# Kernel tuning notes

Measured on AMD Instinct MI355X. Metric: run time of the kernel, lower is better.

## Reference

```python
import jax, jax.numpy as jnp
import numpy as np

EMB = 1024
NHEAD = 16
HEAD_DIM = EMB // NHEAD  # 64
L = 2048
NEG = -1e30


def setup_inputs() -> dict:
    key = jax.random.key(0)
    ks = jax.random.split(key, 8)
    # xavier_uniform bound for square [EMB, EMB] matrices
    bound = float(np.sqrt(6.0 / (EMB + EMB)))
    def xavier(k):
        return jax.random.uniform(k, (EMB, EMB), jnp.float32, -bound, bound)
    return {
        "q": jax.random.normal(ks[0], (L, EMB), jnp.float32),
        "k": jax.random.normal(ks[1], (L, EMB), jnp.float32),
        "v": jax.random.normal(ks[2], (L, EMB), jnp.float32),
        "mask": jax.random.randint(ks[3], (NHEAD, L, L), 0, 2) > 0,
        "Wq": xavier(ks[4]),
        "Wk": xavier(ks[5]),
        "Wv": xavier(ks[6]),
        "Wo": xavier(ks[7]),
    }


def reference(q, k, v, mask, Wq, Wk, Wv, Wo):
    scaling = HEAD_DIM ** -0.5
    # F.linear(x, W) = x @ W.T ; reshape to [H, L, D]
    Q = (q @ Wq.T).reshape(L, NHEAD, HEAD_DIM).swapaxes(0, 1)
    K = (k @ Wk.T).reshape(L, NHEAD, HEAD_DIM).swapaxes(0, 1)
    V = (v @ Wv.T).reshape(L, NHEAD, HEAD_DIM).swapaxes(0, 1)
    scores = jnp.einsum("hld,hmd->hlm", Q, K) * scaling  # [H, L, L]
    scores = jnp.where(mask, jnp.asarray(NEG, scores.dtype), scores)
    p = jax.nn.softmax(scores, axis=-1)
    # attn_mask=True: multiplicative re-mask after softmax (custom path)
    p = p * (~mask).astype(p.dtype)
    # dropout is a no-op in eval mode
    attn_out = jnp.einsum("hlm,hmd->hld", p, V)  # [H, L, D]
    attn_out = attn_out.swapaxes(0, 1).reshape(L, EMB)
    return attn_out @ Wo.T
```

## Files before the change

kernel.cpp:

```cpp
#include <hip/hip_runtime.h>
#include <stdint.h>

#define EMB   1024
#define NHEAD 16
#define HDIM  64
#define SEQ   2048

typedef unsigned short ushort_t;
typedef unsigned int   uint32;
typedef __attribute__((ext_vector_type(8))) short bfrag;
typedef __attribute__((ext_vector_type(4))) float ffrag;

#define MFMA(a, b, c) __builtin_amdgcn_mfma_f32_16x16x32_bf16((a), (b), (c), 0, 0, 0)

__device__ inline ushort_t f2bf(float f) {
  uint32 u = __float_as_uint(f);
  u += 0x7FFFu + ((u >> 16) & 1u);
  return (ushort_t)(u >> 16);
}
__device__ inline uint32 pack2(float a, float b) {
  return (uint32)f2bf(a) | ((uint32)f2bf(b) << 16);
}

__device__ inline void glds16(const ushort_t* g, ushort_t* l) {
  __builtin_amdgcn_global_load_lds(
      (const __attribute__((address_space(1))) uint32*)(uintptr_t)g,
      (__attribute__((address_space(3))) uint32*)(uintptr_t)l, 16, 0, 0);
}

__global__ void detect_mask_kernel(const uint32* __restrict__ mw, int* __restrict__ flag) {
  uint32 w = mw[threadIdx.x];
  bool is4 = (w == 0u) || (w == 1u) || (w == 0x3F800000u);
  unsigned long long bad = __ballot(!is4);
  if (threadIdx.x == 0) flag[0] = (bad == 0ull) ? 1 : 0;
}

__global__ __launch_bounds__(256) void compress_mask(
    const void* __restrict__ maskp, const int* __restrict__ flag, ushort_t* __restrict__ bm)
{
  size_t t = (size_t)blockIdx.x * 256 + threadIdx.x;
  size_t row = t >> 7;
  int c16 = (int)(t & 127);
  size_t base = row * SEQ + (size_t)c16 * 16;
  ushort_t mv = 0;
  if (*flag) {
    const uint4* p = (const uint4*)((const uint32*)maskp + base);
    uint4 a0 = p[0], a1 = p[1], a2 = p[2], a3 = p[3];
    uint32 aw[16] = {a0.x,a0.y,a0.z,a0.w, a1.x,a1.y,a1.z,a1.w,
                     a2.x,a2.y,a2.z,a2.w, a3.x,a3.y,a3.z,a3.w};
    #pragma unroll
    for (int i = 0; i < 16; ++i) mv |= (ushort_t)((aw[i] != 0u) ? 1u : 0u) << i;
  } else {
    uint4 b0 = *(const uint4*)((const unsigned char*)maskp + base);
    uint32 bw[4] = {b0.x, b0.y, b0.z, b0.w};
    #pragma unroll
    for (int i = 0; i < 16; ++i)
      mv |= (ushort_t)((((bw[i >> 2] >> ((i & 3) * 8)) & 0xFFu) != 0u) ? 1u : 0u) << i;
  }
  bm[t] = mv;
}

__global__ __launch_bounds__(256) void cvt_all(
    const float4* __restrict__ q,  const float4* __restrict__ k,  const float4* __restrict__ v,
    const float4* __restrict__ wq, const float4* __restrict__ wk, const float4* __restrict__ wv,
    const float4* __restrict__ wo,
    uint2* __restrict__ qb,  uint2* __restrict__ kb,  uint2* __restrict__ vb,
    uint2* __restrict__ wqb, uint2* __restrict__ wkb, uint2* __restrict__ wvb,
    uint2* __restrict__ wob)
{
  int t = blockIdx.x * 256 + threadIdx.x;
  int s = blockIdx.y;
  const float4* src; uint2* dst; int n4;
  switch (s) {
    case 0: src = q;  dst = qb;  n4 = (SEQ * EMB) / 4; break;
    case 1: src = k;  dst = kb;  n4 = (SEQ * EMB) / 4; break;
    case 2: src = v;  dst = vb;  n4 = (SEQ * EMB) / 4; break;
    case 3: src = wq; dst = wqb; n4 = (EMB * EMB) / 4; break;
    case 4: src = wk; dst = wkb; n4 = (EMB * EMB) / 4; break;
    case 5: src = wv; dst = wvb; n4 = (EMB * EMB) / 4; break;
    default: src = wo; dst = wob; n4 = (EMB * EMB) / 4; break;
  }
  if (t >= n4) return;
  float4 f = src[t];
  uint2 o; o.x = pack2(f.x, f.y); o.y = pack2(f.z, f.w);
  dst[t] = o;
}

template<int MODE, int BN>
__device__ inline void gemm_body(const ushort_t* A, const ushort_t* B, void* Cp,
                                 int m0, int n0, ushort_t* As, ushort_t* Bs) {
  const int tid = threadIdx.x, lane = tid & 63, w = tid >> 6;
  const int wm = (w >> 1) * 64, wn = (w & 1) * (BN / 2);
  const int col = lane & 15, g = lane >> 4;
  constexpr int TN = BN / 32;
  constexpr int BIT = BN / 32;
  constexpr int ASZ = 128 * 64;
  constexpr int BSZ = BN * 64;

  ffrag acc[4][TN] = {};

  auto stage = [&](int kt, int buf) {
    const int k0 = kt * 64;
    ushort_t* Ad = As + buf * ASZ;
    ushort_t* Bd = Bs + buf * BSZ;
    #pragma unroll
    for (int it = 0; it < 4; ++it) {
      int p = it * 256 + tid;
      int row = p >> 3, pc = p & 7;
      glds16(A + (size_t)(m0 + row) * EMB + k0 + (pc ^ (row & 7)) * 8, &Ad[p * 8]);
    }
    #pragma unroll
    for (int it = 0; it < BIT; ++it) {
      int p = it * 256 + tid;
      int row = p >> 3, pc = p & 7;
      glds16(B + (size_t)(n0 + row) * EMB + k0 + (pc ^ (row & 7)) * 8, &Bd[p * 8]);
    }
  };

  stage(0, 0);

  for (int kt = 0; kt < 16; ++kt) {
    const int buf = kt & 1;
    __syncthreads();
    if (kt < 15) stage(kt + 1, buf ^ 1);

    const ushort_t* Ac = As + buf * ASZ;
    const ushort_t* Bc = Bs + buf * BSZ;

    #pragma unroll
    for (int c = 0; c < 2; ++c) {
      bfrag av[4], bv[TN];
      #pragma unroll
      for (int t = 0; t < 4; ++t) {
        int ra = wm + t * 16 + col;
        av[t] = *(const bfrag*)&Ac[ra * 64 + ((c * 4 + g) ^ (ra & 7)) * 8];
      }
      #pragma unroll
      for (int t = 0; t < TN; ++t) {
        int rb = wn + t * 16 + col;
        bv[t] = *(const bfrag*)&Bc[rb * 64 + ((c * 4 + g) ^ (rb & 7)) * 8];
      }
      #pragma unroll
      for (int tm = 0; tm < 4; ++tm)
        #pragma unroll
        for (int tn = 0; tn < TN; ++tn)
          acc[tm][tn] = MFMA(av[tm], bv[tn], acc[tm][tn]);
    }
  }

  const int rbase = g * 4;
  #pragma unroll
  for (int tm = 0; tm < 4; ++tm)
    #pragma unroll
    for (int tn = 0; tn < TN; ++tn)
      #pragma unroll
      for (int r = 0; r < 4; ++r) {
        int m = m0 + wm + tm * 16 + rbase + r;
        int n = n0 + wn + tn * 16 + col;
        float vv = acc[tm][tn][r];
        if (MODE == 0) {
          ((ushort_t*)Cp)[((size_t)(n >> 6) * SEQ + m) * HDIM + (n & 63)] = f2bf(vv);
        } else if (MODE == 1) {
          ((ushort_t*)Cp)[((size_t)(m >> 6) * HDIM + (m & 63)) * SEQ + n] = f2bf(vv);
        } else {
          ((float*)Cp)[(size_t)m * EMB + n] = vv;
        }
      }
}

__global__ __launch_bounds__(256) void gemm_qkv(
    const ushort_t* __restrict__ qb, const ushort_t* __restrict__ kb, const ushort_t* __restrict__ vb,
    const ushort_t* __restrict__ Wqb, const ushort_t* __restrict__ Wkb, const ushort_t* __restrict__ Wvb,
    ushort_t* __restrict__ Qb, ushort_t* __restrict__ Kb, ushort_t* __restrict__ Vtb)
{
  __shared__ ushort_t As[2 * 128 * 64];
  __shared__ ushort_t Bs[2 * 64 * 64];
  const int z = blockIdx.y, bid = blockIdx.x;
  if (z == 0) {
    gemm_body<0, 64>(qb, Wqb, Qb, (bid >> 4) * 128, (bid & 15) * 64, As, Bs);
  } else if (z == 1) {
    gemm_body<0, 64>(kb, Wkb, Kb, (bid >> 4) * 128, (bid & 15) * 64, As, Bs);
  } else {
    gemm_body<1, 64>(Wvb, vb, Vtb, (bid >> 5) * 128, (bid & 31) * 64, As, Bs);
  }
}

__global__ __launch_bounds__(256) void gemm_out(
    const ushort_t* __restrict__ A, const ushort_t* __restrict__ B, float* __restrict__ C)
{
  __shared__ ushort_t As[2 * 128 * 64];
  __shared__ ushort_t Bs[2 * 64 * 64];
  gemm_body<2, 64>(A, B, (void*)C, blockIdx.y * 128, blockIdx.x * 64, As, Bs);
}

__global__ __launch_bounds__(256) void attn_mfma(
    const ushort_t* __restrict__ Qb,
    const ushort_t* __restrict__ Kb,
    const ushort_t* __restrict__ Vtb,
    const ushort_t* __restrict__ bm,
    ushort_t* __restrict__ attnb)
{
  __shared__ ushort_t Ks[2][2][64 * 64];
  __shared__ ushort_t Vs[2][64 * 64];
  __shared__ ushort_t Ps[4][16 * 72];

  const int tid  = threadIdx.x;
  const int lane = tid & 63;
  const int w    = tid >> 6;
  const int h    = blockIdx.y;
  const int l0   = blockIdx.x * 64;
  const int col  = lane & 15, g = lane >> 4, kg8 = g * 8, rbase = g * 4;

  ushort_t* pw = &Ps[w][0];

  {
    int rl = lane >> 2, seg = (lane & 3) * 16;
    const uint4* pq = (const uint4*)(Qb + ((size_t)h * SEQ + l0 + w * 16 + rl) * HDIM + seg);
    uint4 q0 = pq[0], q1 = pq[1];
    *(uint4*)&pw[rl * 72 + seg] = q0;
    *(uint4*)&pw[rl * 72 + seg + 8] = q1;
  }
  bfrag qf[2];
  qf[0] = *(const bfrag*)&pw[col * 72 + kg8];
  qf[1] = *(const bfrag*)&pw[col * 72 + 32 + kg8];

  auto stage_k = [&](int t2, int buf) {
    const int cb = t2 * 128;
    #pragma unroll
    for (int it = 0; it < 2; ++it) {
      int p = it * 256 + tid;
      int row = p >> 3, pc = p & 7;
      int sc = (pc ^ (row & 7)) * 8;
      glds16(Kb + ((size_t)h * SEQ + cb + row) * HDIM + sc,      &Ks[buf][0][p * 8]);
      glds16(Kb + ((size_t)h * SEQ + cb + 64 + row) * HDIM + sc, &Ks[buf][1][p * 8]);
    }
  };
  auto stage_v = [&](int t2) {
    const int cb = t2 * 128;
    #pragma unroll
    for (int it = 0; it < 2; ++it) {
      int p = it * 256 + tid;
      int row = p >> 3, pc = p & 7;
      int sc = (pc ^ (row & 7)) * 8;
      glds16(Vtb + ((size_t)h * HDIM + row) * SEQ + cb + sc,      &Vs[0][p * 8]);
      glds16(Vtb + ((size_t)h * HDIM + row) * SEQ + cb + 64 + sc, &Vs[1][p * 8]);
    }
  };

  stage_k(0, 0);
  stage_v(0);
  __syncthreads();

  const size_t bmbase = ((size_t)h * SEQ + l0 + w * 16 + col) * 128 + g;
  ushort_t mvn0 = bm[bmbase];
  ushort_t mvn1 = bm[bmbase + 4];

  float lsum = 0.f;
  ffrag oacc[4] = {};

  for (int t = 0; t < 16; ++t) {
    const int buf = t & 1;
    if (t < 15) stage_k(t + 1, buf ^ 1);

    int mv0 = (int)mvn0, mv1 = (int)mvn1;
    if (t < 15) {
      mvn0 = bm[bmbase + (size_t)(t + 1) * 8];
      mvn1 = bm[bmbase + (size_t)(t + 1) * 8 + 4];
    }

    ffrag s0[4] = {}, s1[4] = {};
    #pragma unroll
    for (int c = 0; c < 2; ++c)
      #pragma unroll
      for (int tn = 0; tn < 4; ++tn) {
        int row = tn * 16 + col;
        int sw = ((c * 4 + g) ^ (row & 7)) * 8;
        bfrag kf0 = *(const bfrag*)&Ks[buf][0][row * 64 + sw];
        bfrag kf1 = *(const bfrag*)&Ks[buf][1][row * 64 + sw];
        s0[tn] = MFMA(kf0, qf[c], s0[tn]);
        s1[tn] = MFMA(kf1, qf[c], s1[tn]);
      }

    #pragma unroll
    for (int tn = 0; tn < 4; ++tn) {
      int m16 = __shfl(mv0, tn * 16 + col, 64);
      float p0 = ((m16 >> (rbase + 0)) & 1) ? 0.f : __expf(s0[tn][0] * 0.125f);
      float p1 = ((m16 >> (rbase + 1)) & 1) ? 0.f : __expf(s0[tn][1] * 0.125f);
      float p2 = ((m16 >> (rbase + 2)) & 1) ? 0.f : __expf(s0[tn][2] * 0.125f);
      float p3 = ((m16 >> (rbase + 3)) & 1) ? 0.f : __expf(s0[tn][3] * 0.125f);
      lsum += (p0 + p1) + (p2 + p3);
      uint2 pk; pk.x = pack2(p0, p1); pk.y = pack2(p2, p3);
      *(uint2*)&pw[col * 72 + tn * 16 + rbase] = pk;
    }

    __syncthreads();

    #pragma unroll
    for (int c = 0; c < 2; ++c) {
      bfrag af = *(const bfrag*)&pw[col * 72 + c * 32 + kg8];
      #pragma unroll
      for (int tn = 0; tn < 4; ++tn) {
        int row = tn * 16 + col;
        bfrag vf = *(const bfrag*)&Vs[0][row * 64 + ((c * 4 + g) ^ (row & 7)) * 8];
        oacc[tn] = MFMA(af, vf, oacc[tn]);
      }
    }

    #pragma unroll
    for (int tn = 0; tn < 4; ++tn) {
      int m16 = __shfl(mv1, tn * 16 + col, 64);
      float p0 = ((m16 >> (rbase + 0)) & 1) ? 0.f : __expf(s1[tn][0] * 0.125f);
      float p1 = ((m16 >> (rbase + 1)) & 1) ? 0.f : __expf(s1[tn][1] * 0.125f);
      float p2 = ((m16 >> (rbase + 2)) & 1) ? 0.f : __expf(s1[tn][2] * 0.125f);
      float p3 = ((m16 >> (rbase + 3)) & 1) ? 0.f : __expf(s1[tn][3] * 0.125f);
      lsum += (p0 + p1) + (p2 + p3);
      uint2 pk; pk.x = pack2(p0, p1); pk.y = pack2(p2, p3);
      *(uint2*)&pw[col * 72 + tn * 16 + rbase] = pk;
    }

    #pragma unroll
    for (int c = 0; c < 2; ++c) {
      bfrag af = *(const bfrag*)&pw[col * 72 + c * 32 + kg8];
      #pragma unroll
      for (int tn = 0; tn < 4; ++tn) {
        int row = tn * 16 + col;
        bfrag vf = *(const bfrag*)&Vs[1][row * 64 + ((c * 4 + g) ^ (row & 7)) * 8];
        oacc[tn] = MFMA(af, vf, oacc[tn]);
      }
    }

    __syncthreads();
    if (t < 15) stage_v(t + 1);
  }

  float s_ = lsum;
  s_ += __shfl_xor(s_, 16, 64);
  s_ += __shfl_xor(s_, 32, 64);
  float invf = (s_ > 0.f) ? (1.0f / s_) : 0.0f;
  float inv[4];
  #pragma unroll
  for (int r = 0; r < 4; ++r) inv[r] = __shfl(invf, rbase + r, 64);

  #pragma unroll
  for (int tn = 0; tn < 4; ++tn)
    #pragma unroll
    for (int r = 0; r < 4; ++r) {
      int qg = l0 + w * 16 + rbase + r;
      attnb[(size_t)qg * EMB + h * HDIM + tn * 16 + col] = f2bf(oacc[tn][r] * inv[r]);
    }
}

extern "C" void kernel_launch(void* const* d_in, const int* in_sizes, int n_in,
                              void* d_out, int out_size, void* d_ws, size_t ws_size,
                              hipStream_t stream) {
  const float* q    = (const float*)d_in[0];
  const float* k    = (const float*)d_in[1];
  const float* v    = (const float*)d_in[2];
  const void*  mask =               d_in[3];
  const float* Wq   = (const float*)d_in[4];
  const float* Wk   = (const float*)d_in[5];
  const float* Wv   = (const float*)d_in[6];
  const float* Wo   = (const float*)d_in[7];

  char* ws = (char*)d_ws;
  const size_t MB = 1024 * 1024;
  ushort_t* qb    = (ushort_t*)(ws);
  ushort_t* kb    = (ushort_t*)(ws + 4  * MB);
  ushort_t* vb    = (ushort_t*)(ws + 8  * MB);
  ushort_t* Wqb   = (ushort_t*)(ws + 12 * MB);
  ushort_t* Wkb   = (ushort_t*)(ws + 14 * MB);
  ushort_t* Wvb   = (ushort_t*)(ws + 16 * MB);
  ushort_t* Wob   = (ushort_t*)(ws + 18 * MB);
  ushort_t* Qb    = (ushort_t*)(ws + 20 * MB);
  ushort_t* Kb    = (ushort_t*)(ws + 24 * MB);
  ushort_t* Vtb   = (ushort_t*)(ws + 28 * MB);
  int*      flag  = (int*)     (ws + 32 * MB);
  ushort_t* bmask = (ushort_t*)(ws + 33 * MB);
  ushort_t* attnb = qb;

  detect_mask_kernel<<<1, 64, 0, stream>>>((const uint32*)mask, flag);

  compress_mask<<<16384, 256, 0, stream>>>(mask, flag, bmask);

  cvt_all<<<dim3((SEQ * EMB / 4 + 255) / 256, 7), 256, 0, stream>>>(
      (const float4*)q, (const float4*)k, (const float4*)v,
      (const float4*)Wq, (const float4*)Wk, (const float4*)Wv, (const float4*)Wo,
      (uint2*)qb, (uint2*)kb, (uint2*)vb,
      (uint2*)Wqb, (uint2*)Wkb, (uint2*)Wvb, (uint2*)Wob);

  gemm_qkv<<<dim3(256, 3), 256, 0, stream>>>(qb, kb, vb, Wqb, Wkb, Wvb, Qb, Kb, Vtb);

  attn_mfma<<<dim3(SEQ / 64, NHEAD), 256, 0, stream>>>(Qb, Kb, Vtb, bmask, attnb);

  gemm_out<<<dim3(16, 16), 256, 0, stream>>>(attnb, Wob, (float*)d_out);
}
```

Measured before the change: 468.9 us.

## Fuse mask reading into attention kernel and restructure to 64-key tiles

Drops the separate mask-detect and mask-compress kernels. The attention kernel now detects the mask format itself and reads the raw mask directly, prefetching one tile ahead. The main loop changes from 16 steps of 128 keys to 32 steps of 64 keys, with K and V double-buffered together and one barrier per step instead of two. This saves a full pass over the 64M-element mask and two launches. In exchange, the attention kernel reads the uncompressed mask (bytes or 32-bit words) with less contiguous per-lane loads, and the loop runs twice as many iterations.

After: 447.2 us. 1.05x faster.

```diff
diff --git a/kernel.cpp b/kernel.cpp
--- a/kernel.cpp
+++ b/kernel.cpp
@@ -26,38 +26,6 @@
   __builtin_amdgcn_global_load_lds(
       (const __attribute__((address_space(1))) uint32*)(uintptr_t)g,
       (__attribute__((address_space(3))) uint32*)(uintptr_t)l, 16, 0, 0);
-}
-
-__global__ void detect_mask_kernel(const uint32* __restrict__ mw, int* __restrict__ flag) {
-  uint32 w = mw[threadIdx.x];
-  bool is4 = (w == 0u) || (w == 1u) || (w == 0x3F800000u);
-  unsigned long long bad = __ballot(!is4);
-  if (threadIdx.x == 0) flag[0] = (bad == 0ull) ? 1 : 0;
-}
-
-__global__ __launch_bounds__(256) void compress_mask(
-    const void* __restrict__ maskp, const int* __restrict__ flag, ushort_t* __restrict__ bm)
-{
-  size_t t = (size_t)blockIdx.x * 256 + threadIdx.x;
-  size_t row = t >> 7;
-  int c16 = (int)(t & 127);
-  size_t base = row * SEQ + (size_t)c16 * 16;
-  ushort_t mv = 0;
-  if (*flag) {
-    const uint4* p = (const uint4*)((const uint32*)maskp + base);
-    uint4 a0 = p[0], a1 = p[1], a2 = p[2], a3 = p[3];
-    uint32 aw[16] = {a0.x,a0.y,a0.z,a0.w, a1.x,a1.y,a1.z,a1.w,
-                     a2.x,a2.y,a2.z,a2.w, a3.x,a3.y,a3.z,a3.w};
-    #pragma unroll
-    for (int i = 0; i < 16; ++i) mv |= (ushort_t)((aw[i] != 0u) ? 1u : 0u) << i;
-  } else {
-    uint4 b0 = *(const uint4*)((const unsigned char*)maskp + base);
-    uint32 bw[4] = {b0.x, b0.y, b0.z, b0.w};
-    #pragma unroll
-    for (int i = 0; i < 16; ++i)
-      mv |= (ushort_t)((((bw[i >> 2] >> ((i & 3) * 8)) & 0xFFu) != 0u) ? 1u : 0u) << i;
-  }
-  bm[t] = mv;
 }
 
 __global__ __launch_bounds__(256) void cvt_all(
@@ -197,10 +165,10 @@
     const ushort_t* __restrict__ Qb,
     const ushort_t* __restrict__ Kb,
     const ushort_t* __restrict__ Vtb,
-    const ushort_t* __restrict__ bm,
+    const void*    __restrict__ maskp,
     ushort_t* __restrict__ attnb)
 {
-  __shared__ ushort_t Ks[2][2][64 * 64];
+  __shared__ ushort_t Ks[2][64 * 64];
   __shared__ ushort_t Vs[2][64 * 64];
   __shared__ ushort_t Ps[4][16 * 72];
 
@@ -211,6 +179,10 @@
   const int l0   = blockIdx.x * 64;
   const int col  = lane & 15, g = lane >> 4, kg8 = g * 8, rbase = g * 4;
 
+  uint32 mw0 = ((const uint32*)maskp)[lane];
+  bool is4 = (mw0 == 0u) || (mw0 == 1u) || (mw0 == 0x3F800000u);
+  const bool flag4 = (__ballot(!is4) == 0ull);
+
   ushort_t* pw = &Ps[w][0];
 
   {
@@ -224,113 +196,87 @@
   qf[0] = *(const bfrag*)&pw[col * 72 + kg8];
   qf[1] = *(const bfrag*)&pw[col * 72 + 32 + kg8];
 
-  auto stage_k = [&](int t2, int buf) {
-    const int cb = t2 * 128;
+  auto stage = [&](int t2, int b) {
+    const int cb = t2 * 64;
     #pragma unroll
     for (int it = 0; it < 2; ++it) {
       int p = it * 256 + tid;
       int row = p >> 3, pc = p & 7;
       int sc = (pc ^ (row & 7)) * 8;
-      glds16(Kb + ((size_t)h * SEQ + cb + row) * HDIM + sc,      &Ks[buf][0][p * 8]);
-      glds16(Kb + ((size_t)h * SEQ + cb + 64 + row) * HDIM + sc, &Ks[buf][1][p * 8]);
+      glds16(Kb  + ((size_t)h * SEQ + cb + row) * HDIM + sc, &Ks[b][p * 8]);
+      glds16(Vtb + ((size_t)h * HDIM + row) * SEQ + cb + sc, &Vs[b][p * 8]);
     }
   };
-  auto stage_v = [&](int t2) {
-    const int cb = t2 * 128;
-    #pragma unroll
-    for (int it = 0; it < 2; ++it) {
-      int p = it * 256 + tid;
-      int row = p >> 3, pc = p & 7;
-      int sc = (pc ^ (row & 7)) * 8;
-      glds16(Vtb + ((size_t)h * HDIM + row) * SEQ + cb + sc,      &Vs[0][p * 8]);
-      glds16(Vtb + ((size_t)h * HDIM + row) * SEQ + cb + 64 + sc, &Vs[1][p * 8]);
+
+  const size_t mrow = (size_t)h * SEQ + l0 + w * 16 + col;
+  uint4 mn[4], mc[4];
+  auto load_mask = [&](int t2) {
+    const int cb = t2 * 64 + rbase;
+    if (flag4) {
+      const uint32* m32 = (const uint32*)maskp + mrow * SEQ + cb;
+      #pragma unroll
+      for (int tn = 0; tn < 4; ++tn) mn[tn] = *(const uint4*)(m32 + tn * 16);
+    } else {
+      const unsigned char* m8 = (const unsigned char*)maskp + mrow * SEQ + cb;
+      #pragma unroll
+      for (int tn = 0; tn < 4; ++tn) {
+        uint32 b4 = *(const uint32*)(m8 + tn * 16);
+        mn[tn].x = b4 & 0xFFu; mn[tn].y = (b4 >> 8) & 0xFFu;
+        mn[tn].z = (b4 >> 16) & 0xFFu; mn[tn].w = b4 >> 24;
+      }
     }
   };
 
-  stage_k(0, 0);
-  stage_v(0);
+  stage(0, 0);
+  load_mask(0);
   __syncthreads();
-
-  const size_t bmbase = ((size_t)h * SEQ + l0 + w * 16 + col) * 128 + g;
-  ushort_t mvn0 = bm[bmbase];
-  ushort_t mvn1 = bm[bmbase + 4];
 
   float lsum = 0.f;
   ffrag oacc[4] = {};
 
-  for (int t = 0; t < 16; ++t) {
+  for (int t = 0; t < 32; ++t) {
     const int buf = t & 1;
-    if (t < 15) stage_k(t + 1, buf ^ 1);
-
-    int mv0 = (int)mvn0, mv1 = (int)mvn1;
-    if (t < 15) {
-      mvn0 = bm[bmbase + (size_t)(t + 1) * 8];
-      mvn1 = bm[bmbase + (size_t)(t + 1) * 8 + 4];
-    }
-
-    ffrag s0[4] = {}, s1[4] = {};
+
+    #pragma unroll
+    for (int tn = 0; tn < 4; ++tn) mc[tn] = mn[tn];
+    if (t < 31) {
+      stage(t + 1, buf ^ 1);
+      load_mask(t + 1);
+    }
+
+    ffrag s[4] = {};
     #pragma unroll
     for (int c = 0; c < 2; ++c)
       #pragma unroll
       for (int tn = 0; tn < 4; ++tn) {
         int row = tn * 16 + col;
-        int sw = ((c * 4 + g) ^ (row & 7)) * 8;
-        bfrag kf0 = *(const bfrag*)&Ks[buf][0][row * 64 + sw];
-        bfrag kf1 = *(const bfrag*)&Ks[buf][1][row * 64 + sw];
-        s0[tn] = MFMA(kf0, qf[c], s0[tn]);
-        s1[tn] = MFMA(kf1, qf[c], s1[tn]);
+        bfrag kf = *(const bfrag*)&Ks[buf][row * 64 + ((c * 4 + g) ^ (row & 7)) * 8];
+        s[tn] = MFMA(kf, qf[c], s[tn]);
       }
 
     #pragma unroll
     for (int tn = 0; tn < 4; ++tn) {
-      int m16 = __shfl(mv0, tn * 16 + col, 64);
-      float p0 = ((m16 >> (rbase + 0)) & 1) ? 0.f : __expf(s0[tn][0] * 0.125f);
-      float p1 = ((m16 >> (rbase + 1)) & 1) ? 0.f : __expf(s0[tn][1] * 0.125f);
-      float p2 = ((m16 >> (rbase + 2)) & 1) ? 0.f : __expf(s0[tn][2] * 0.125f);
-      float p3 = ((m16 >> (rbase + 3)) & 1) ? 0.f : __expf(s0[tn][3] * 0.125f);
+      float p0 = mc[tn].x ? 0.f : __expf(s[tn][0] * 0.125f);
+      float p1 = mc[tn].y ? 0.f : __expf(s[tn][1] * 0.125f);
+      float p2 = mc[tn].z ? 0.f : __expf(s[tn][2] * 0.125f);
+      float p3 = mc[tn].w ? 0.f : __expf(s[tn][3] * 0.125f);
       lsum += (p0 + p1) + (p2 + p3);
       uint2 pk; pk.x = pack2(p0, p1); pk.y = pack2(p2, p3);
       *(uint2*)&pw[col * 72 + tn * 16 + rbase] = pk;
     }
 
-    __syncthreads();
-
     #pragma unroll
     for (int c = 0; c < 2; ++c) {
       bfrag af = *(const bfrag*)&pw[col * 72 + c * 32 + kg8];
       #pragma unroll
       for (int tn = 0; tn < 4; ++tn) {
         int row = tn * 16 + col;
-        bfrag vf = *(const bfrag*)&Vs[0][row * 64 + ((c * 4 + g) ^ (row & 7)) * 8];
+        bfrag vf = *(const bfrag*)&Vs[buf][row * 64 + ((c * 4 + g) ^ (row & 7)) * 8];
         oacc[tn] = MFMA(af, vf, oacc[tn]);
       }
     }
 
-    #pragma unroll
-    for (int tn = 0; tn < 4; ++tn) {
-      int m16 = __shfl(mv1, tn * 16 + col, 64);
-      float p0 = ((m16 >> (rbase + 0)) & 1) ? 0.f : __expf(s1[tn][0] * 0.125f);
-      float p1 = ((m16 >> (rbase + 1)) & 1) ? 0.f : __expf(s1[tn][1] * 0.125f);
-      float p2 = ((m16 >> (rbase + 2)) & 1) ? 0.f : __expf(s1[tn][2] * 0.125f);
-      float p3 = ((m16 >> (rbase + 3)) & 1) ? 0.f : __expf(s1[tn][3] * 0.125f);
-      lsum += (p0 + p1) + (p2 + p3);
-      uint2 pk; pk.x = pack2(p0, p1); pk.y = pack2(p2, p3);
-      *(uint2*)&pw[col * 72 + tn * 16 + rbase] = pk;
-    }
-
-    #pragma unroll
-    for (int c = 0; c < 2; ++c) {
-      bfrag af = *(const bfrag*)&pw[col * 72 + c * 32 + kg8];
-      #pragma unroll
-      for (int tn = 0; tn < 4; ++tn) {
-        int row = tn * 16 + col;
-        bfrag vf = *(const bfrag*)&Vs[1][row * 64 + ((c * 4 + g) ^ (row & 7)) * 8];
-        oacc[tn] = MFMA(af, vf, oacc[tn]);
-      }
-    }
-
     __syncthreads();
-    if (t < 15) stage_v(t + 1);
   }
 
   float s_ = lsum;
@@ -374,13 +320,7 @@
   ushort_t* Qb    = (ushort_t*)(ws + 20 * MB);
   ushort_t* Kb    = (ushort_t*)(ws + 24 * MB);
   ushort_t* Vtb   = (ushort_t*)(ws + 28 * MB);
-  int*      flag  = (int*)     (ws + 32 * MB);
-  ushort_t* bmask = (ushort_t*)(ws + 33 * MB);
   ushort_t* attnb = qb;
-
-  detect_mask_kernel<<<1, 64, 0, stream>>>((const uint32*)mask, flag);
-
-  compress_mask<<<16384, 256, 0, stream>>>(mask, flag, bmask);
 
   cvt_all<<<dim3((SEQ * EMB / 4 + 255) / 256, 7), 256, 0, stream>>>(
       (const float4*)q, (const float4*)k, (const float4*)v,
@@ -390,7 +330,7 @@
 
   gemm_qkv<<<dim3(256, 3), 256, 0, stream>>>(qb, kb, vb, Wqb, Wkb, Wvb, Qb, Kb, Vtb);
 
-  attn_mfma<<<dim3(SEQ / 64, NHEAD), 256, 0, stream>>>(Qb, Kb, Vtb, bmask, attnb);
+  attn_mfma<<<dim3(SEQ / 64, NHEAD), 256, 0, stream>>>(Qb, Kb, Vtb, mask, attnb);
 
   gemm_out<<<dim3(16, 16), 256, 0, stream>>>(attnb, Wob, (float*)d_out);
 }
```
